# Kernel optimization log

Hardware: AMD Instinct MI355X
Metric: run time of the kernel (lower is better)

The kernel has to match this reference:

```python
import jax, jax.numpy as jnp
import numpy as np

N_NODES = 100000


def _gcn_norm(edge_index, num_nodes):
    # PyG GCNConv default: add self-loops, symmetric normalization
    src, dst = edge_index[0], edge_index[1]
    loop = jnp.arange(num_nodes, dtype=src.dtype)
    src = jnp.concatenate([src, loop])
    dst = jnp.concatenate([dst, loop])
    deg = jax.ops.segment_sum(jnp.ones_like(dst, dtype=jnp.float32), dst,
                              num_segments=num_nodes)
    dinv = jnp.where(deg > 0, jax.lax.rsqrt(deg), 0.0)
    norm = dinv[src] * dinv[dst]  # [E + N]
    return src, dst, norm


def _gcn_conv(x, W, b, src, dst, norm, num_nodes):
    h = x @ W                                   # [N, out] linear first (PyG)
    msg = h[src] * norm[:, None]                # gather + scale  [E+N, out]
    out = jax.ops.segment_sum(msg, dst, num_segments=num_nodes)  # scatter-add
    return out + b


def setup_inputs() -> dict:
    key = jax.random.key(0)
    ks = jax.random.split(key, 5)
    x = jax.random.normal(ks[0], (N_NODES, 3), dtype=jnp.float32)
    edge_index = jax.random.randint(ks[1], (2, 1600000), 0, N_NODES, dtype=jnp.int64)
    # Glorot-ish weights, zero bias (PyG defaults)
    W1 = jax.random.normal(ks[2], (3, 64), dtype=jnp.float32) * (1.0 / np.sqrt(3))
    W2 = jax.random.normal(ks[3], (64, 64), dtype=jnp.float32) * (1.0 / np.sqrt(64))
    W3 = jax.random.normal(ks[4], (64, 3), dtype=jnp.float32) * (1.0 / np.sqrt(64))
    b1 = jnp.zeros((64,), jnp.float32)
    b2 = jnp.zeros((64,), jnp.float32)
    b3 = jnp.zeros((3,), jnp.float32)
    return {"x": x, "edge_index": edge_index, "W1": W1, "b1": b1,
            "W2": W2, "b2": b2, "W3": W3, "b3": b3}


def reference(x, edge_index, W1, b1, W2, b2, W3, b3):
    n = x.shape[0]
    src, dst, norm = _gcn_norm(edge_index, n)  # same graph for every layer
    h = jax.nn.relu(_gcn_conv(x, W1, b1, src, dst, norm, n))
    h = jax.nn.relu(_gcn_conv(h, W2, b2, src, dst, norm, n))
    return _gcn_conv(h, W3, b3, src, dst, norm, n)
```

## Files before the change

### kernel.cpp

```cpp
#include <hip/hip_runtime.h>

#define TPB 256
#define NB 391
#define CH 4096
#define BS 4736


__device__ __forceinline__ unsigned bpack(float a, float b) {
    unsigned ua = __float_as_uint(a), ub = __float_as_uint(b);
    ua = (ua + 0x7fffu + ((ua >> 16) & 1u)) >> 16;
    ub = (ub + 0x7fffu + ((ub >> 16) & 1u)) >> 16;
    return ua | (ub << 16);
}
__device__ __forceinline__ float blo(unsigned u) { return __uint_as_float(u << 16); }
__device__ __forceinline__ float bhi(unsigned u) { return __uint_as_float(u & 0xffff0000u); }


__global__ __launch_bounds__(512) void k_init(unsigned* __restrict__ gcur) {
    int t = threadIdx.x;
    if (t < NB) gcur[t] = (unsigned)(t * BS);
}


__global__ __launch_bounds__(TPB) void k_placeA(const int* __restrict__ src,
                                                const int* __restrict__ dst,
                                                unsigned* __restrict__ gcur,
                                                unsigned* __restrict__ bkt, int E) {
    __shared__ unsigned val[CH];
    __shared__ unsigned dstS[CH];
    __shared__ unsigned short bid[CH];
    __shared__ unsigned cnt[512], loff[512], lcur[512], basev[512];
    __shared__ unsigned tsum[TPB];
    int t = threadIdx.x;
    int c0 = blockIdx.x * CH;
    int n = E - c0; if (n > CH) n = CH;

    for (int b = t; b < 512; b += TPB) { cnt[b] = 0; lcur[b] = 0; }
    __syncthreads();
    for (int i = t; i < n; i += TPB) {
        unsigned d = (unsigned)dst[c0 + i];
        dstS[i] = d;
        atomicAdd(&cnt[d >> 8], 1u);
    }
    __syncthreads();
    for (int b = t; b < NB; b += TPB)
        basev[b] = cnt[b] ? atomicAdd(&gcur[b], cnt[b]) : 0u;
    unsigned a0 = cnt[2 * t], a1 = cnt[2 * t + 1];
    tsum[t] = a0 + a1;
    __syncthreads();
#pragma unroll
    for (int o = 1; o < TPB; o <<= 1) {
        unsigned v = (t >= o) ? tsum[t - o] : 0u;
        __syncthreads();
        tsum[t] += v;
        __syncthreads();
    }
    unsigned ex = tsum[t] - (a0 + a1);
    loff[2 * t] = ex; loff[2 * t + 1] = ex + a0;
    __syncthreads();
    for (int i = t; i < n; i += TPB) {
        unsigned s = (unsigned)src[c0 + i];
        unsigned d = dstS[i];
        unsigned b = d >> 8;
        unsigned r = atomicAdd(&lcur[b], 1u);
        unsigned slot = loff[b] + r;
        val[slot] = s | ((d & 255u) << 20);
        bid[slot] = (unsigned short)b;
    }
    __syncthreads();
    for (int i = t; i < n; i += TPB) {
        unsigned b = bid[i];
        bkt[basev[b] + ((unsigned)i - loff[b])] = val[i];
    }
}


__global__ __launch_bounds__(512) void k_fineS(const unsigned* __restrict__ bkt,
                                               const unsigned* __restrict__ gcur,
                                               const float* __restrict__ x,
                                               int2* __restrict__ rp2,
                                               int* __restrict__ ssrc,
                                               float* __restrict__ dinv,
                                               float4* __restrict__ xs4, int N) {
    __shared__ unsigned cnt[256], sc[256], off[256];
    __shared__ unsigned bs[BS];
    int t = threadIdx.x, b = blockIdx.x;
    if (t < 256) cnt[t] = 0;
    __syncthreads();
    int p0 = b * BS, p1 = (int)gcur[b];
    int n = p1 - p0;
    for (int i = t; i < n; i += 512) {
        unsigned u = bkt[p0 + i];
        bs[i] = u;
        atomicAdd(&cnt[u >> 20], 1u);
    }
    __syncthreads();
    unsigned c = (t < 256) ? cnt[t] : 0u;
    if (t < 256) sc[t] = c;
    __syncthreads();
#pragma unroll
    for (int o = 1; o < 256; o <<= 1) {
        unsigned v = (t >= o && t < 256) ? sc[t - o] : 0u;
        __syncthreads();
        if (t < 256) sc[t] += v;
        __syncthreads();
    }
    if (t < 256) {
        unsigned ex = sc[t] - c;
        off[t] = (unsigned)p0 + ex;
        int node = (b << 8) + t;
        if (node < N) {
            int beg = p0 + (int)ex;
            rp2[node] = make_int2(beg, beg + (int)c);
            float dv = rsqrtf((float)(c + 1u));
            dinv[node] = dv;
            float4 xv;
            xv.x = x[node * 3 + 0] * dv;
            xv.y = x[node * 3 + 1] * dv;
            xv.z = x[node * 3 + 2] * dv;
            xv.w = 0.f;
            xs4[node] = xv;
        }
    }
    __syncthreads();
    for (int i = t; i < n; i += 512) {
        unsigned u = bs[i];
        unsigned r = atomicAdd(&off[u >> 20], 1u);
        ssrc[r] = (int)(u & 0xFFFFFu);
    }
}


__global__ __launch_bounds__(TPB) void k_l1q(const float* __restrict__ xs4,
                                             const int2* __restrict__ rp2,
                                             const int* __restrict__ ssrc,
                                             const float* __restrict__ dinv,
                                             const float* __restrict__ W1,
                                             const float* __restrict__ b1,
                                             const float* __restrict__ W2,
                                             uint4* __restrict__ gb, int N) {
    __shared__ float Ws[4096];
    for (int i = threadIdx.x; i < 4096; i += TPB) Ws[i] = W2[i];
    __syncthreads();
    int tid = blockIdx.x * TPB + threadIdx.x;
    int node = tid >> 2, c = tid & 3;
    if (node >= N) return;
    int2 r = rp2[node];
    float acc = xs4[tid];
    int j = r.x;
    for (; j + 3 < r.y; j += 4) {
        int s0 = ssrc[j], s1 = ssrc[j+1], s2 = ssrc[j+2], s3 = ssrc[j+3];
        acc += (xs4[(s0 << 2) + c] + xs4[(s1 << 2) + c])
             + (xs4[(s2 << 2) + c] + xs4[(s3 << 2) + c]);
    }
    for (; j < r.y; ++j) acc += xs4[(ssrc[j] << 2) + c];
    float dv = dinv[node];
    acc *= dv;
    int base = (threadIdx.x & 63) & ~3;
    float q0 = __shfl(acc, base + 0, 64);
    float q1 = __shfl(acc, base + 1, 64);
    float q2 = __shfl(acc, base + 2, 64);

    float o[16];
#pragma unroll
    for (int i = 0; i < 16; ++i) o[i] = 0.f;
    const int cofs = c << 4;
    for (int kb = 0; kb < 16; ++kb) {
        int k0 = __builtin_amdgcn_readfirstlane(kb) << 2;
        const float* W1k = W1 + k0;
        const float* b1k = b1 + k0;
        float h[4];
        h[0] = fmaxf(fmaf(q0, W1k[0], fmaf(q1, W1k[64], fmaf(q2, W1k[128], b1k[0]))), 0.f);
        h[1] = fmaxf(fmaf(q0, W1k[1], fmaf(q1, W1k[65], fmaf(q2, W1k[129], b1k[1]))), 0.f);
        h[2] = fmaxf(fmaf(q0, W1k[2], fmaf(q1, W1k[66], fmaf(q2, W1k[130], b1k[2]))), 0.f);
        h[3] = fmaxf(fmaf(q0, W1k[3], fmaf(q1, W1k[67], fmaf(q2, W1k[131], b1k[3]))), 0.f);
#pragma unroll
        for (int kk = 0; kk < 4; ++kk) {
            const float4* Wp = (const float4*)(Ws + ((k0 + kk) << 6) + cofs);
#pragma unroll
            for (int ii = 0; ii < 4; ++ii) {
                float4 w = Wp[ii];
                o[4*ii+0] = fmaf(h[kk], w.x, o[4*ii+0]);
                o[4*ii+1] = fmaf(h[kk], w.y, o[4*ii+1]);
                o[4*ii+2] = fmaf(h[kk], w.z, o[4*ii+2]);
                o[4*ii+3] = fmaf(h[kk], w.w, o[4*ii+3]);
            }
        }
    }
    uint4 v0, v1;
    v0.x = bpack(o[0] * dv,  o[1] * dv);
    v0.y = bpack(o[2] * dv,  o[3] * dv);
    v0.z = bpack(o[4] * dv,  o[5] * dv);
    v0.w = bpack(o[6] * dv,  o[7] * dv);
    v1.x = bpack(o[8] * dv,  o[9] * dv);
    v1.y = bpack(o[10] * dv, o[11] * dv);
    v1.z = bpack(o[12] * dv, o[13] * dv);
    v1.w = bpack(o[14] * dv, o[15] * dv);
    uint4* gp = gb + ((size_t)node << 3) + (c << 1);
    gp[0] = v0;
    gp[1] = v1;
}


__global__ __launch_bounds__(TPB) void k_p2fb(const uint4* __restrict__ gb,
                                              const int2* __restrict__ rp2,
                                              const int* __restrict__ ssrc,
                                              const float* __restrict__ dinv,
                                              const float* __restrict__ b2,
                                              const float* __restrict__ W3,
                                              float* __restrict__ q4, int N) {
    int tid = blockIdx.x * TPB + threadIdx.x;
    int node = tid >> 3, q = tid & 7;
    if (node >= N) return;
    int2 r = rp2[node];
    int beg = r.x, end = r.y;
    float a[8];
    {
        uint4 u = gb[((size_t)node << 3) + q];
        a[0] = blo(u.x); a[1] = bhi(u.x);
        a[2] = blo(u.y); a[3] = bhi(u.y);
        a[4] = blo(u.z); a[5] = bhi(u.z);
        a[6] = blo(u.w); a[7] = bhi(u.w);
    }
    int j = beg;
    for (; j + 3 < end; j += 4) {
        int s0 = ssrc[j], s1 = ssrc[j+1], s2 = ssrc[j+2], s3 = ssrc[j+3];
        uint4 u0 = gb[((size_t)s0 << 3) + q];
        uint4 u1 = gb[((size_t)s1 << 3) + q];
        uint4 u2 = gb[((size_t)s2 << 3) + q];
        uint4 u3 = gb[((size_t)s3 << 3) + q];
        a[0] += (blo(u0.x) + blo(u1.x)) + (blo(u2.x) + blo(u3.x));
        a[1] += (bhi(u0.x) + bhi(u1.x)) + (bhi(u2.x) + bhi(u3.x));
        a[2] += (blo(u0.y) + blo(u1.y)) + (blo(u2.y) + blo(u3.y));
        a[3] += (bhi(u0.y) + bhi(u1.y)) + (bhi(u2.y) + bhi(u3.y));
        a[4] += (blo(u0.z) + blo(u1.z)) + (blo(u2.z) + blo(u3.z));
        a[5] += (bhi(u0.z) + bhi(u1.z)) + (bhi(u2.z) + bhi(u3.z));
        a[6] += (blo(u0.w) + blo(u1.w)) + (blo(u2.w) + blo(u3.w));
        a[7] += (bhi(u0.w) + bhi(u1.w)) + (bhi(u2.w) + bhi(u3.w));
    }
    for (; j < end; ++j) {
        uint4 u = gb[((size_t)ssrc[j] << 3) + q];
        a[0] += blo(u.x); a[1] += bhi(u.x);
        a[2] += blo(u.y); a[3] += bhi(u.y);
        a[4] += blo(u.z); a[5] += bhi(u.z);
        a[6] += blo(u.w); a[7] += bhi(u.w);
    }
    float dv = dinv[node];
    int f0 = q << 3;
    const float* bb = b2 + f0;
    const float* Wr = W3 + f0 * 3;
    float p0 = 0.f, p1 = 0.f, p2 = 0.f;
#pragma unroll
    for (int i = 0; i < 8; ++i) {
        float h = fmaxf(fmaf(a[i], dv, bb[i]), 0.f);
        p0 = fmaf(h, Wr[3*i+0], p0);
        p1 = fmaf(h, Wr[3*i+1], p1);
        p2 = fmaf(h, Wr[3*i+2], p2);
    }
#pragma unroll
    for (int off = 1; off < 8; off <<= 1) {
        p0 += __shfl_xor(p0, off, 64);
        p1 += __shfl_xor(p1, off, 64);
        p2 += __shfl_xor(p2, off, 64);
    }
    if (q < 4) {
        float v = (q == 0) ? p0 * dv : (q == 1) ? p1 * dv : (q == 2) ? p2 * dv : 0.f;
        q4[((size_t)node << 2) + q] = v;
    }
}


__global__ __launch_bounds__(TPB) void k_pull3o(const float* __restrict__ g34,
                                                const int2* __restrict__ rp2,
                                                const int* __restrict__ ssrc,
                                                const float* __restrict__ dinv,
                                                const float* __restrict__ b3,
                                                float* __restrict__ out, int N) {
    int tid = blockIdx.x * TPB + threadIdx.x;
    int node = tid >> 2, c = tid & 3;
    if (node >= N) return;
    int2 r = rp2[node];
    int beg = r.x, end = r.y;
    float acc = g34[tid];
    int j = beg;
    for (; j + 3 < end; j += 4) {
        int s0 = ssrc[j], s1 = ssrc[j+1], s2 = ssrc[j+2], s3 = ssrc[j+3];
        acc += (g34[(s0 << 2) + c] + g34[(s1 << 2) + c])
             + (g34[(s2 << 2) + c] + g34[(s3 << 2) + c]);
    }
    for (; j < end; ++j) acc += g34[(ssrc[j] << 2) + c];
    if (c < 3) out[(size_t)node * 3 + c] = dinv[node] * acc + b3[c];
}

extern "C" void kernel_launch(void* const* d_in, const int* in_sizes, int n_in,
                              void* d_out, int out_size, void* d_ws, size_t ws_size,
                              hipStream_t stream) {
    const float* x  = (const float*)d_in[0];
    const int*   ei = (const int*)  d_in[1];
    const float* W1 = (const float*)d_in[2];
    const float* b1 = (const float*)d_in[3];
    const float* W2 = (const float*)d_in[4];
    const float* b2 = (const float*)d_in[5];
    const float* W3 = (const float*)d_in[6];
    const float* b3 = (const float*)d_in[7];
    float* out = (float*)d_out;

    const int N = in_sizes[0] / 3;
    const int E = in_sizes[1] / 2;
    const int* srcI = ei;
    const int* dstI = ei + E;

    float*    ws   = (float*)d_ws;
    unsigned* gcur = (unsigned*)ws;
    int2*     rp2  = (int2*)    (ws + 512);
    float*    dinv = ws + 512 + 2 * (size_t)N;
    int*      ssrc = (int*)     (dinv + N);
    float*    xs4  = (float*)(ssrc + (size_t)NB * BS + 4);
    float*    q4   = xs4 + (size_t)N * 4;
    unsigned* gb   = (unsigned*)(q4 + (size_t)N * 4);
    unsigned* bkt  = gb + (size_t)N * 32;

    int gPlace = (E + CH - 1) / CH;
    int gS3    = (N * 4 + TPB - 1) / TPB;
    int gP2    = (int)(((size_t)N * 8 + TPB - 1) / TPB);

    k_init  <<<1,      512, 0, stream>>>(gcur);
    k_placeA<<<gPlace, TPB, 0, stream>>>(srcI, dstI, gcur, bkt, E);
    k_fineS <<<NB,     512, 0, stream>>>(bkt, gcur, x, rp2, ssrc, dinv,
                                         (float4*)xs4, N);

    k_l1q<<<gS3, TPB, 0, stream>>>(xs4, rp2, ssrc, dinv,
                                   W1, b1, W2, (uint4*)gb, N);

    k_p2fb<<<gP2, TPB, 0, stream>>>((const uint4*)gb, rp2, ssrc, dinv,
                                    b2, W3, q4, N);

    k_pull3o<<<gS3, TPB, 0, stream>>>(q4, rp2, ssrc, dinv, b3, out, N);
}
```

Measured before the change: 208.9 us.

## Restructure layer-1 kernel: two-phase aggregate then per-half-feature GEMV from global weights

The layer-1 kernel now handles 128 nodes per block. It first aggregates the 3-channel features into shared memory over two rounds. Then each thread computes 32 of the 64 output features for one node, reading W2 directly from global with uniform addresses (scalar loads) instead of staging it in LDS. This removes the per-block 16 KB LDS fill and barrier, but raises register pressure from o[32]. Index loads of ssrc in the three gather kernels and the q4 store are switched to nontemporal hints.

```diff
diff --git a/kernel.cpp b/kernel.cpp
--- a/kernel.cpp
+++ b/kernel.cpp
@@ -131,7 +131,7 @@
 }
 
 
-__global__ __launch_bounds__(TPB) void k_l1q(const float* __restrict__ xs4,
+__global__ __launch_bounds__(TPB) void k_l1s(const float* __restrict__ xs4,
                                              const int2* __restrict__ rp2,
                                              const int* __restrict__ ssrc,
                                              const float* __restrict__ dinv,
@@ -139,32 +139,42 @@
                                              const float* __restrict__ b1,
                                              const float* __restrict__ W2,
                                              uint4* __restrict__ gb, int N) {
-    __shared__ float Ws[4096];
-    for (int i = threadIdx.x; i < 4096; i += TPB) Ws[i] = W2[i];
-    __syncthreads();
-    int tid = blockIdx.x * TPB + threadIdx.x;
-    int node = tid >> 2, c = tid & 3;
+    __shared__ float qs[128 * 4];
+    int t = threadIdx.x;
+    int n0 = blockIdx.x << 7;
+#pragma unroll
+    for (int rnd = 0; rnd < 2; ++rnd) {
+        int local = (rnd << 6) + (t >> 2);
+        int node = n0 + local;
+        int c = t & 3;
+        if (node < N) {
+            int2 r = rp2[node];
+            float acc = xs4[(node << 2) + c];
+            int j = r.x;
+            for (; j + 3 < r.y; j += 4) {
+                int s0 = __builtin_nontemporal_load(ssrc + j);
+                int s1 = __builtin_nontemporal_load(ssrc + j + 1);
+                int s2 = __builtin_nontemporal_load(ssrc + j + 2);
+                int s3 = __builtin_nontemporal_load(ssrc + j + 3);
+                acc += (xs4[(s0 << 2) + c] + xs4[(s1 << 2) + c])
+                     + (xs4[(s2 << 2) + c] + xs4[(s3 << 2) + c]);
+            }
+            for (; j < r.y; ++j) acc += xs4[(__builtin_nontemporal_load(ssrc + j) << 2) + c];
+            float dv = dinv[node];
+            qs[(local << 2) + c] = (c < 3) ? acc * dv : dv;
+        }
+    }
+    __syncthreads();
+    int local = t & 127;
+    int half = __builtin_amdgcn_readfirstlane(t >> 7);
+    int node = n0 + local;
     if (node >= N) return;
-    int2 r = rp2[node];
-    float acc = xs4[tid];
-    int j = r.x;
-    for (; j + 3 < r.y; j += 4) {
-        int s0 = ssrc[j], s1 = ssrc[j+1], s2 = ssrc[j+2], s3 = ssrc[j+3];
-        acc += (xs4[(s0 << 2) + c] + xs4[(s1 << 2) + c])
-             + (xs4[(s2 << 2) + c] + xs4[(s3 << 2) + c]);
-    }
-    for (; j < r.y; ++j) acc += xs4[(ssrc[j] << 2) + c];
-    float dv = dinv[node];
-    acc *= dv;
-    int base = (threadIdx.x & 63) & ~3;
-    float q0 = __shfl(acc, base + 0, 64);
-    float q1 = __shfl(acc, base + 1, 64);
-    float q2 = __shfl(acc, base + 2, 64);
-
-    float o[16];
-#pragma unroll
-    for (int i = 0; i < 16; ++i) o[i] = 0.f;
-    const int cofs = c << 4;
+    float4 qv = ((const float4*)qs)[local];
+    float q0 = qv.x, q1 = qv.y, q2 = qv.z, dv = qv.w;
+    float o[32];
+#pragma unroll
+    for (int i = 0; i < 32; ++i) o[i] = 0.f;
+    const int fofs = half << 5;
     for (int kb = 0; kb < 16; ++kb) {
         int k0 = __builtin_amdgcn_readfirstlane(kb) << 2;
         const float* W1k = W1 + k0;
@@ -176,29 +186,22 @@
         h[3] = fmaxf(fmaf(q0, W1k[3], fmaf(q1, W1k[67], fmaf(q2, W1k[131], b1k[3]))), 0.f);
 #pragma unroll
         for (int kk = 0; kk < 4; ++kk) {
-            const float4* Wp = (const float4*)(Ws + ((k0 + kk) << 6) + cofs);
-#pragma unroll
-            for (int ii = 0; ii < 4; ++ii) {
-                float4 w = Wp[ii];
-                o[4*ii+0] = fmaf(h[kk], w.x, o[4*ii+0]);
-                o[4*ii+1] = fmaf(h[kk], w.y, o[4*ii+1]);
-                o[4*ii+2] = fmaf(h[kk], w.z, o[4*ii+2]);
-                o[4*ii+3] = fmaf(h[kk], w.w, o[4*ii+3]);
-            }
+            const float* Wr = W2 + ((k0 + kk) << 6) + fofs;
+#pragma unroll
+            for (int i = 0; i < 32; ++i)
+                o[i] = fmaf(h[kk], Wr[i], o[i]);
         }
     }
-    uint4 v0, v1;
-    v0.x = bpack(o[0] * dv,  o[1] * dv);
-    v0.y = bpack(o[2] * dv,  o[3] * dv);
-    v0.z = bpack(o[4] * dv,  o[5] * dv);
-    v0.w = bpack(o[6] * dv,  o[7] * dv);
-    v1.x = bpack(o[8] * dv,  o[9] * dv);
-    v1.y = bpack(o[10] * dv, o[11] * dv);
-    v1.z = bpack(o[12] * dv, o[13] * dv);
-    v1.w = bpack(o[14] * dv, o[15] * dv);
-    uint4* gp = gb + ((size_t)node << 3) + (c << 1);
-    gp[0] = v0;
-    gp[1] = v1;
+    uint4* gp = gb + ((size_t)node << 3) + (half << 2);
+#pragma unroll
+    for (int g8 = 0; g8 < 4; ++g8) {
+        uint4 v;
+        v.x = bpack(o[8*g8+0] * dv, o[8*g8+1] * dv);
+        v.y = bpack(o[8*g8+2] * dv, o[8*g8+3] * dv);
+        v.z = bpack(o[8*g8+4] * dv, o[8*g8+5] * dv);
+        v.w = bpack(o[8*g8+6] * dv, o[8*g8+7] * dv);
+        gp[g8] = v;
+    }
 }
 
 
@@ -224,7 +227,10 @@
     }
     int j = beg;
     for (; j + 3 < end; j += 4) {
-        int s0 = ssrc[j], s1 = ssrc[j+1], s2 = ssrc[j+2], s3 = ssrc[j+3];
+        int s0 = __builtin_nontemporal_load(ssrc + j);
+        int s1 = __builtin_nontemporal_load(ssrc + j + 1);
+        int s2 = __builtin_nontemporal_load(ssrc + j + 2);
+        int s3 = __builtin_nontemporal_load(ssrc + j + 3);
         uint4 u0 = gb[((size_t)s0 << 3) + q];
         uint4 u1 = gb[((size_t)s1 << 3) + q];
         uint4 u2 = gb[((size_t)s2 << 3) + q];
@@ -239,7 +245,7 @@
         a[7] += (bhi(u0.w) + bhi(u1.w)) + (bhi(u2.w) + bhi(u3.w));
     }
     for (; j < end; ++j) {
-        uint4 u = gb[((size_t)ssrc[j] << 3) + q];
+        uint4 u = gb[((size_t)__builtin_nontemporal_load(ssrc + j) << 3) + q];
         a[0] += blo(u.x); a[1] += bhi(u.x);
         a[2] += blo(u.y); a[3] += bhi(u.y);
         a[4] += blo(u.z); a[5] += bhi(u.z);
@@ -265,7 +271,7 @@
     }
     if (q < 4) {
         float v = (q == 0) ? p0 * dv : (q == 1) ? p1 * dv : (q == 2) ? p2 * dv : 0.f;
-        q4[((size_t)node << 2) + q] = v;
+        __builtin_nontemporal_store(v, q4 + (((size_t)node << 2) + q));
     }
 }
 
@@ -284,11 +290,14 @@
     float acc = g34[tid];
     int j = beg;
     for (; j + 3 < end; j += 4) {
-        int s0 = ssrc[j], s1 = ssrc[j+1], s2 = ssrc[j+2], s3 = ssrc[j+3];
+        int s0 = __builtin_nontemporal_load(ssrc + j);
+        int s1 = __builtin_nontemporal_load(ssrc + j + 1);
+        int s2 = __builtin_nontemporal_load(ssrc + j + 2);
+        int s3 = __builtin_nontemporal_load(ssrc + j + 3);
         acc += (g34[(s0 << 2) + c] + g34[(s1 << 2) + c])
              + (g34[(s2 << 2) + c] + g34[(s3 << 2) + c]);
     }
-    for (; j < end; ++j) acc += g34[(ssrc[j] << 2) + c];
+    for (; j < end; ++j) acc += g34[(__builtin_nontemporal_load(ssrc + j) << 2) + c];
     if (c < 3) out[(size_t)node * 3 + c] = dinv[node] * acc + b3[c];
 }
 
@@ -323,13 +332,14 @@
     int gPlace = (E + CH - 1) / CH;
     int gS3    = (N * 4 + TPB - 1) / TPB;
     int gP2    = (int)(((size_t)N * 8 + TPB - 1) / TPB);
+    int gL1    = (N + 127) / 128;
 
     k_init  <<<1,      512, 0, stream>>>(gcur);
     k_placeA<<<gPlace, TPB, 0, stream>>>(srcI, dstI, gcur, bkt, E);
     k_fineS <<<NB,     512, 0, stream>>>(bkt, gcur, x, rp2, ssrc, dinv,
                                          (float4*)xs4, N);
 
-    k_l1q<<<gS3, TPB, 0, stream>>>(xs4, rp2, ssrc, dinv,
+    k_l1s<<<gL1, TPB, 0, stream>>>(xs4, rp2, ssrc, dinv,
                                    W1, b1, W2, (uint4*)gb, N);
 
     k_p2fb<<<gP2, TPB, 0, stream>>>((const uint4*)gb, rp2, ssrc, dinv,
```

Measured after the change: 218.6 us. +4.7%, slower.
